# Kernel tuning notes

Hardware: AMD Instinct MI355X
Metric: run time of the kernel (lower is better)

Reference implementation:

```python
import jax, jax.numpy as jnp
import numpy as np

H = 4096        # hidden_size
NH = 32         # num query heads
NKV = 8         # num kv heads
D = H // NH     # head_dim = 128
S = 2048        # num tokens (single causal sequence)
THETA = 1000000.0
SCALE = D ** -0.5


def _rope(x, positions):
    # neox-style (rotate-half) RoPE over full head_dim, as vLLM's get_rope default
    half = D // 2
    inv_freq = 1.0 / (THETA ** (jnp.arange(half, dtype=jnp.float32) / half))
    ang = positions.astype(jnp.float32)[:, None] * inv_freq          # [S, D/2]
    cos = jnp.cos(ang)[:, None, :]                                   # [S, 1, D/2]
    sin = jnp.sin(ang)[:, None, :]
    x1, x2 = x[..., :half], x[..., half:]
    return jnp.concatenate([x1 * cos - x2 * sin, x2 * cos + x1 * sin], axis=-1)


def setup_inputs() -> dict:
    key = jax.random.key(0)
    k1, k2, k3 = jax.random.split(key, 3)
    positions = jnp.arange(S, dtype=jnp.int32)
    hidden_states = jax.random.normal(k1, (S, H), dtype=jnp.float32)
    w_qkv = jax.random.normal(k2, ((NH + 2 * NKV) * D, H), dtype=jnp.float32) * 0.02
    w_o = jax.random.normal(k3, (H, NH * D), dtype=jnp.float32) * 0.02
    return {"positions": positions, "hidden_states": hidden_states,
            "w_qkv": w_qkv, "w_o": w_o}


def reference(positions, hidden_states, w_qkv, w_o):
    # fused QKV projection (Linear, bias=False): x @ W^T
    qkv = hidden_states @ w_qkv.T                                    # [S, (NH+2*NKV)*D]
    q, k, v = jnp.split(qkv, [NH * D, (NH + NKV) * D], axis=-1)
    q = q.reshape(S, NH, D)
    k = k.reshape(S, NKV, D)
    v = v.reshape(S, NKV, D)
    # RoPE on q and k
    q = _rope(q, positions)
    k = _rope(k, positions)
    # GQA causal attention: group NH query heads onto NKV kv heads
    g = NH // NKV
    qg = q.reshape(S, NKV, g, D)
    scores = jnp.einsum('qhgd,khd->hgqk', qg, k) * SCALE             # [NKV, g, S, S]
    causal = positions[:, None] >= positions[None, :]                # [S, S]
    scores = jnp.where(causal[None, None], scores, jnp.float32(-1e30))
    probs = jax.nn.softmax(scores, axis=-1)
    o = jnp.einsum('hgqk,khd->qhgd', probs, v).reshape(S, NH * D)
    return o @ w_o.T                                                 # [S, H]
```

## Files before the change

### kernel.cpp

```cpp
#include <hip/hip_runtime.h>
#include <hip/hip_bf16.h>

#define S_LEN 2048
#define HID 4096
#define NH 32
#define NKV 8
#define DH 128
#define QKV_N ((NH + 2 * NKV) * DH)
#define SCALE_ATT 0.08838834764831845f
#define SCALE2_ATT 0.12751744f

typedef __bf16 bf16;
typedef __bf16 bf16x8 __attribute__((ext_vector_type(8)));
typedef __bf16 bf16x4 __attribute__((ext_vector_type(4)));
typedef float f32x4 __attribute__((ext_vector_type(4)));
typedef float f32x16 __attribute__((ext_vector_type(16)));

__device__ inline f32x4 mfma16(bf16x8 a, bf16x8 b, f32x4 c) {
    return __builtin_amdgcn_mfma_f32_16x16x32_bf16(a, b, c, 0, 0, 0);
}
__device__ inline f32x16 mfma32(bf16x8 a, bf16x8 b, f32x16 c) {
    return __builtin_amdgcn_mfma_f32_32x32x16_bf16(a, b, c, 0, 0, 0);
}

__device__ inline bf16x8 load8(const float* p) {
    const float4 a = ((const float4*)p)[0];
    const float4 b = ((const float4*)p)[1];
    bf16x8 r;
    r[0] = (bf16)a.x; r[1] = (bf16)a.y; r[2] = (bf16)a.z; r[3] = (bf16)a.w;
    r[4] = (bf16)b.x; r[5] = (bf16)b.y; r[6] = (bf16)b.z; r[7] = (bf16)b.w;
    return r;
}
__device__ inline bf16x8 load8(const bf16* p) { return *(const bf16x8*)p; }

__device__ inline void load_lds16(const bf16* g, bf16* lds_base) {
    __builtin_amdgcn_global_load_lds(
        (const __attribute__((address_space(1))) void*)g,
        (__attribute__((address_space(3))) void*)lds_base, 16, 0, 0);
}

__device__ inline unsigned pack2_bf16(float lo, float hi) {
    union { bf16 h[2]; unsigned u; } r;
    r.h[0] = (bf16)lo;
    r.h[1] = (bf16)hi;
    return r.u;
}

__global__ __launch_bounds__(256) void cvt_kernel(const float* __restrict__ src,
                                                  bf16* __restrict__ dst, int n8) {
    int i = blockIdx.x * 256 + threadIdx.x;
    if (i >= n8) return;
    *(bf16x8*)&dst[(size_t)i * 8] = load8(&src[(size_t)i * 8]);
}

template <typename OutT>
__global__ __launch_bounds__(256) void gemm_bt_swz(const bf16* __restrict__ A,
                                                   const bf16* __restrict__ B,
                                                   OutT* __restrict__ C,
                                                   int K, int lda, int ldc) {
    const int tid = threadIdx.x;
    const int lane = tid & 63;
    const int w = tid >> 6;
    const int m0 = blockIdx.y * 128;
    const int n0 = blockIdx.x * 128;
    const int wm = (w >> 1) * 64;
    const int wn = (w & 1) * 64;
    const int ln = lane & 15;
    const int qo = lane >> 4;

    __shared__ bf16 As[128 * 64];
    __shared__ bf16 Bs[128 * 64];

    const int rseg = lane >> 3;
    const int gc = (lane & 7) ^ (rseg & 7);

    f32x4 acc[4][4];
#pragma unroll
    for (int mi = 0; mi < 4; ++mi)
#pragma unroll
        for (int ni = 0; ni < 4; ++ni) acc[mi][ni] = f32x4{0.f, 0.f, 0.f, 0.f};

    for (int k0 = 0; k0 < K; k0 += 64) {
#pragma unroll
        for (int j = 0; j < 4; ++j) {
            const int seg = w * 4 + j;
            const int r = seg * 8 + rseg;
            load_lds16(&A[(size_t)(m0 + r) * lda + k0 + gc * 8], &As[seg * 512]);
            load_lds16(&B[(size_t)(n0 + r) * K + k0 + gc * 8], &Bs[seg * 512]);
        }
        __syncthreads();
#pragma unroll
        for (int kk = 0; kk < 2; ++kk) {
            bf16x8 af[4], bfr[4];
#pragma unroll
            for (int mi = 0; mi < 4; ++mi) {
                const int m = wm + mi * 16 + ln;
                const int sc = (kk * 4 + qo) ^ (ln & 7);
                af[mi] = *(const bf16x8*)&As[m * 64 + sc * 8];
            }
#pragma unroll
            for (int ni = 0; ni < 4; ++ni) {
                const int n = wn + ni * 16 + ln;
                const int sc = (kk * 4 + qo) ^ (ln & 7);
                bfr[ni] = *(const bf16x8*)&Bs[n * 64 + sc * 8];
            }
#pragma unroll
            for (int mi = 0; mi < 4; ++mi)
#pragma unroll
                for (int ni = 0; ni < 4; ++ni)
                    acc[mi][ni] = mfma16(af[mi], bfr[ni], acc[mi][ni]);
        }
        __syncthreads();
    }
#pragma unroll
    for (int mi = 0; mi < 4; ++mi)
#pragma unroll
        for (int ni = 0; ni < 4; ++ni)
#pragma unroll
            for (int r = 0; r < 4; ++r) {
                int row = m0 + wm + mi * 16 + qo * 4 + r;
                int col = n0 + wn + ni * 16 + ln;
                C[(size_t)row * ldc + col] = (OutT)acc[mi][ni][r];
            }
}

template <typename AT, typename OutT>
__global__ __launch_bounds__(256) void gemm_bt(const AT* __restrict__ A,
                                               const float* __restrict__ B,
                                               OutT* __restrict__ C,
                                               int K, int lda, int ldc) {
    const int tid = threadIdx.x;
    const int lane = tid & 63;
    const int w = tid >> 6;
    const int m0 = blockIdx.y * 128;
    const int n0 = blockIdx.x * 128;
    const int wm = (w >> 1) * 64;
    const int wn = (w & 1) * 64;
    const int ln = lane & 15;
    const int qo = lane >> 4;

    __shared__ bf16 As[128 * 72];
    __shared__ bf16 Bs[128 * 72];

    f32x4 acc[4][4];
#pragma unroll
    for (int mi = 0; mi < 4; ++mi)
#pragma unroll
        for (int ni = 0; ni < 4; ++ni) acc[mi][ni] = f32x4{0.f, 0.f, 0.f, 0.f};

    for (int k0 = 0; k0 < K; k0 += 64) {
#pragma unroll
        for (int i = 0; i < 4; ++i) {
            int v = tid + i * 256;
            int row = v >> 3;
            int col = (v & 7) * 8;
            *(bf16x8*)&As[row * 72 + col] = load8(&A[(size_t)(m0 + row) * lda + k0 + col]);
            *(bf16x8*)&Bs[row * 72 + col] = load8(&B[(size_t)(n0 + row) * K + k0 + col]);
        }
        __syncthreads();
#pragma unroll
        for (int kk = 0; kk < 64; kk += 32) {
            bf16x8 af[4], bfr[4];
#pragma unroll
            for (int mi = 0; mi < 4; ++mi)
                af[mi] = *(const bf16x8*)&As[(wm + mi * 16 + ln) * 72 + kk + qo * 8];
#pragma unroll
            for (int ni = 0; ni < 4; ++ni)
                bfr[ni] = *(const bf16x8*)&Bs[(wn + ni * 16 + ln) * 72 + kk + qo * 8];
#pragma unroll
            for (int mi = 0; mi < 4; ++mi)
#pragma unroll
                for (int ni = 0; ni < 4; ++ni)
                    acc[mi][ni] = mfma16(af[mi], bfr[ni], acc[mi][ni]);
        }
        __syncthreads();
    }
#pragma unroll
    for (int mi = 0; mi < 4; ++mi)
#pragma unroll
        for (int ni = 0; ni < 4; ++ni)
#pragma unroll
            for (int r = 0; r < 4; ++r) {
                int row = m0 + wm + mi * 16 + qo * 4 + r;
                int col = n0 + wn + ni * 16 + ln;
                C[(size_t)row * ldc + col] = (OutT)acc[mi][ni][r];
            }
}

__global__ __launch_bounds__(256) void rope_kernel(bf16* __restrict__ qkv,
                                                   const int* __restrict__ positions) {
    int idx = blockIdx.x * 256 + threadIdx.x;
    const int total = S_LEN * (NH + NKV) * 64;
    if (idx >= total) return;
    int d = idx & 63;
    int t = idx >> 6;
    int head = t % (NH + NKV);
    int s = t / (NH + NKV);
    size_t base = (size_t)s * QKV_N + (head < NH ? head * DH : NH * DH + (head - NH) * DH);
    float x1 = (float)qkv[base + d];
    float x2 = (float)qkv[base + d + 64];
    float pos = (float)positions[s];
    float inv = expf(-0.21586735246819178f * (float)d);
    float ang = pos * inv;
    float c = cosf(ang);
    float sn = sinf(ang);
    qkv[base + d] = (bf16)(x1 * c - x2 * sn);
    qkv[base + d + 64] = (bf16)(x2 * c + x1 * sn);
}

__global__ __launch_bounds__(256) void vtrans_kernel(const bf16* __restrict__ qkv,
                                                     bf16* __restrict__ vt_g) {
    const int tid = threadIdx.x;
    const int s0 = blockIdx.x * 64;
    const int kvh = blockIdx.y;
    __shared__ bf16 Ls[64 * 136];
#pragma unroll
    for (int i = 0; i < 4; ++i) {
        int v = tid + i * 256;
        int row = v >> 4;
        int col = (v & 15) * 8;
        *(bf16x8*)&Ls[row * 136 + col] =
            *(const bf16x8*)&qkv[(size_t)(s0 + row) * QKV_N + (NH + NKV) * DH + kvh * DH + col];
    }
    __syncthreads();
#pragma unroll
    for (int i = 0; i < 4; ++i) {
        int u = tid + i * 256;
        int d = u >> 3;
        int sg = (u & 7) * 8;
        bf16x8 r;
#pragma unroll
        for (int j = 0; j < 8; ++j) r[j] = Ls[(sg + j) * 136 + d];
        *(bf16x8*)&vt_g[((size_t)kvh * DH + d) * S_LEN + s0 + sg] = r;
    }
}

__global__ __launch_bounds__(256) void attn_kernel(bf16* __restrict__ qkv,
                                                   const bf16* __restrict__ vt_g) {
    const int tid = threadIdx.x;
    const int lane = tid & 63;
    const int w = tid >> 6;
    const int ln = lane & 31;
    const int hi = lane >> 5;
    const int hq = blockIdx.x;
    const int qtile = (int)gridDim.y - 1 - (int)blockIdx.y;
    const int kvh = hq >> 2;
    const int q0 = qtile * 128;
    const int qrow = q0 + w * 32 + ln;

    __shared__ __align__(128) bf16 Ks[2][64 * 128];
    __shared__ __align__(128) bf16 Vt[2][128 * 64];

    bf16x8 qf[8];
    {
        const bf16* qptr = qkv + (size_t)qrow * QKV_N + hq * DH + hi * 8;
#pragma unroll
        for (int s = 0; s < 8; ++s) qf[s] = *(const bf16x8*)(qptr + s * 16);
    }

    const bf16* ksrc = qkv + NH * DH + kvh * DH;
    const bf16* vsrc = vt_g + (size_t)kvh * DH * S_LEN;
    const int kcK = lane & 15;
    const int krs = lane >> 4;
    const int kcV = lane & 7;
    const int vrs = lane >> 3;

    auto stage = [&](int buf, int kt) {
        const int k0s = kt * 64;
#pragma unroll
        for (int j = 0; j < 4; ++j) {
            int r = w * 16 + j * 4 + krs;
            load_lds16(ksrc + (size_t)(k0s + r) * QKV_N + ((kcK ^ (r & 7)) * 8),
                       &Ks[buf][(w * 16 + j * 4) * 128]);
        }
#pragma unroll
        for (int j = 0; j < 4; ++j) {
            int d = w * 32 + j * 8 + vrs;
            load_lds16(vsrc + (size_t)d * S_LEN + k0s + ((kcV ^ (d & 7)) * 8),
                       &Vt[buf][(w * 32 + j * 8) * 64]);
        }
    };

    f32x16 acc[4];
#pragma unroll
    for (int t = 0; t < 4; ++t)
#pragma unroll
        for (int r = 0; r < 16; ++r) acc[t][r] = 0.f;
    float m2 = -1e30f, l = 0.f;

    const int kt_last = (q0 + 127) >> 6;
    int buf = 0;
    stage(0, 0);
    __syncthreads();

    for (int kt = 0; kt <= kt_last; ++kt) {
        if (kt < kt_last) stage(buf ^ 1, kt + 1);
        const int k0 = kt * 64;
        if (k0 <= q0 + w * 32 + 31) {
            f32x16 st[2];
#pragma unroll
            for (int t = 0; t < 2; ++t)
#pragma unroll
                for (int r = 0; r < 16; ++r) st[t][r] = 0.f;
            const bf16* Kb = &Ks[buf][0];
            __builtin_amdgcn_s_setprio(1);
#pragma unroll
            for (int t = 0; t < 2; ++t) {
                const int key = t * 32 + ln;
#pragma unroll
                for (int s = 0; s < 8; ++s) {
                    bf16x8 kf =
                        *(const bf16x8*)&Kb[key * 128 + (((2 * s + hi) ^ (key & 7)) * 8)];
                    st[t] = mfma32(kf, qf[s], st[t]);
                }
            }
            __builtin_amdgcn_s_setprio(0);
            const bool needMask = (k0 + 63 > q0 + w * 32);
            float tmax = -1e30f;
#pragma unroll
            for (int t = 0; t < 2; ++t)
#pragma unroll
                for (int r = 0; r < 16; ++r) {
                    int kcol = k0 + t * 32 + (r & 3) + 8 * (r >> 2) + 4 * hi;
                    float v = st[t][r] * SCALE2_ATT;
                    if (needMask && kcol > qrow) v = -1e30f;
                    st[t][r] = v;
                    tmax = fmaxf(tmax, v);
                }
            tmax = fmaxf(tmax, __shfl_xor(tmax, 32, 64));
            float mnew = fmaxf(m2, tmax);
            float alpha = exp2f(m2 - mnew);
            float rs = 0.f;
#pragma unroll
            for (int t = 0; t < 2; ++t)
#pragma unroll
                for (int r = 0; r < 16; ++r) {
                    float e = exp2f(st[t][r] - mnew);
                    st[t][r] = e;
                    rs += e;
                }
            rs += __shfl_xor(rs, 32, 64);
            l = l * alpha + rs;
            m2 = mnew;
#pragma unroll
            for (int t = 0; t < 4; ++t)
#pragma unroll
                for (int r = 0; r < 16; ++r) acc[t][r] *= alpha;
            unsigned cw[16];
#pragma unroll
            for (int i = 0; i < 16; ++i)
                cw[i] = pack2_bf16(st[i >> 3][2 * (i & 7)], st[i >> 3][2 * (i & 7) + 1]);
            bf16x8 pa[4];
#pragma unroll
            for (int ks = 0; ks < 4; ++ks) {
                const int base = (ks >> 1) * 8 + (ks & 1) * 4;
                union { unsigned u[4]; bf16x8 v; } pk;
#pragma unroll
                for (int e = 0; e < 2; ++e) {
                    unsigned A = cw[base + e];
                    unsigned B = cw[base + 2 + e];
                    unsigned tA = (unsigned)__shfl_xor((int)A, 32, 64);
                    unsigned tB = (unsigned)__shfl_xor((int)B, 32, 64);
                    pk.u[e] = hi ? tB : A;
                    pk.u[e + 2] = hi ? B : tA;
                }
                pa[ks] = pk.v;
            }
            const bf16* Vb = &Vt[buf][0];
            __builtin_amdgcn_s_setprio(1);
#pragma unroll
            for (int dt = 0; dt < 4; ++dt) {
                const int d = dt * 32 + ln;
#pragma unroll
                for (int ks = 0; ks < 4; ++ks) {
                    bf16x8 vf =
                        *(const bf16x8*)&Vb[d * 64 + (((2 * ks + hi) ^ (d & 7)) * 8)];
                    acc[dt] = mfma32(vf, pa[ks], acc[dt]);
                }
            }
            __builtin_amdgcn_s_setprio(0);
        }
        __syncthreads();
        buf ^= 1;
    }

    const float invl = 1.f / l;
    bf16* outp = qkv + (size_t)qrow * QKV_N + hq * DH;
#pragma unroll
    for (int dt = 0; dt < 4; ++dt)
#pragma unroll
        for (int rq = 0; rq < 4; ++rq) {
            bf16x4 o;
#pragma unroll
            for (int i = 0; i < 4; ++i) o[i] = (bf16)(acc[dt][rq * 4 + i] * invl);
            *(bf16x4*)(outp + dt * 32 + rq * 8 + hi * 4) = o;
        }
}

extern "C" void kernel_launch(void* const* d_in, const int* in_sizes, int n_in,
                              void* d_out, int out_size, void* d_ws, size_t ws_size,
                              hipStream_t stream) {
    const int* positions = (const int*)d_in[0];
    const float* hidden = (const float*)d_in[1];
    const float* w_qkv = (const float*)d_in[2];
    const float* w_o = (const float*)d_in[3];
    float* out = (float*)d_out;

    const size_t n_qkv = (size_t)S_LEN * QKV_N;
    const size_t n_vt = (size_t)NKV * DH * S_LEN;
    const size_t n_hid = (size_t)S_LEN * HID;
    const size_t n_wqkv = (size_t)QKV_N * HID;
    const size_t n_wo = (size_t)HID * HID;

    const size_t need_min = (n_qkv + n_vt) * sizeof(bf16);
    const size_t need_full = (n_qkv + n_vt + n_hid + n_wqkv + n_wo) * sizeof(bf16);
    if (ws_size < need_min) return;

    bf16* qkv = (bf16*)d_ws;
    bf16* vt_g = qkv + n_qkv;
    bf16* hid_b = vt_g + n_vt;
    bf16* wqkv_b = hid_b + n_hid;
    bf16* wo_b = wqkv_b + n_wqkv;
    const bool full = ws_size >= need_full;

    if (full) {
        cvt_kernel<<<(int)(n_hid / 8 + 255) / 256, 256, 0, stream>>>(hidden, hid_b, (int)(n_hid / 8));
        cvt_kernel<<<(int)(n_wqkv / 8 + 255) / 256, 256, 0, stream>>>(w_qkv, wqkv_b, (int)(n_wqkv / 8));
        cvt_kernel<<<(int)(n_wo / 8 + 255) / 256, 256, 0, stream>>>(w_o, wo_b, (int)(n_wo / 8));
        gemm_bt_swz<<<dim3(QKV_N / 128, S_LEN / 128), 256, 0, stream>>>(hid_b, wqkv_b, qkv, HID, HID, QKV_N);
    } else {
        gemm_bt<<<dim3(QKV_N / 128, S_LEN / 128), 256, 0, stream>>>(hidden, w_qkv, qkv, HID, HID, QKV_N);
    }
    const int total = S_LEN * (NH + NKV) * 64;
    rope_kernel<<<(total + 255) / 256, 256, 0, stream>>>(qkv, positions);
    vtrans_kernel<<<dim3(S_LEN / 64, NKV), 256, 0, stream>>>(qkv, vt_g);
    attn_kernel<<<dim3(NH, S_LEN / 128), 256, 0, stream>>>(qkv, vt_g);
    if (full) {
        gemm_bt_swz<<<dim3(HID / 128, S_LEN / 128), 256, 0, stream>>>(qkv, wo_b, out, HID, QKV_N, HID);
    } else {
        gemm_bt<<<dim3(HID / 128, S_LEN / 128), 256, 0, stream>>>(qkv, w_o, out, HID, QKV_N, HID);
    }
}
```

Measured before the change: 551.0 us.

## Replace bf16 GEMMs with larger double-buffered 512-thread 32x32 MFMA kernel

Replaces the 128x128 single-buffered GEMM used for the QKV and output projections with a 256xBN tile kernel of 512 threads. It double-buffers LDS with async global-to-LDS loads and explicit vmcnt waits, uses 32x32x16 MFMAs, and remaps workgroups so neighbouring blocks share data. The intent is to overlap memory loads with MFMA work and raise arithmetic intensity per tile. In exchange it uses much more dynamic LDS (96-128 KB), which may limit occupancy, and the hand-tuned waitcnt counts have to match the number of issued loads.

```diff
diff --git a/kernel.cpp b/kernel.cpp
--- a/kernel.cpp
+++ b/kernel.cpp
@@ -53,74 +53,121 @@
     *(bf16x8*)&dst[(size_t)i * 8] = load8(&src[(size_t)i * 8]);
 }
 
-template <typename OutT>
-__global__ __launch_bounds__(256) void gemm_bt_swz(const bf16* __restrict__ A,
+template <int BN, typename OutT>
+__global__ __launch_bounds__(512, 2) void gemm_8ph(const bf16* __restrict__ A,
                                                    const bf16* __restrict__ B,
                                                    OutT* __restrict__ C,
                                                    int K, int lda, int ldc) {
+    constexpr int WTN = BN / 4;
+    constexpr int NREP = WTN / 32;
+    constexpr int BLOADS = BN / 64;
+    extern __shared__ char smem[];
+    bf16* As = (bf16*)smem;
+    bf16* Bs = (bf16*)(smem + 2 * 256 * 64 * 2);
+
     const int tid = threadIdx.x;
     const int lane = tid & 63;
     const int w = tid >> 6;
-    const int m0 = blockIdx.y * 128;
-    const int n0 = blockIdx.x * 128;
-    const int wm = (w >> 1) * 64;
-    const int wn = (w & 1) * 64;
-    const int ln = lane & 15;
-    const int qo = lane >> 4;
-
-    __shared__ bf16 As[128 * 64];
-    __shared__ bf16 Bs[128 * 64];
-
+    const int wm = w >> 2;
+    const int wn = w & 3;
+    const int ln = lane & 31;
+    const int hi = lane >> 5;
     const int rseg = lane >> 3;
-    const int gc = (lane & 7) ^ (rseg & 7);
-
-    f32x4 acc[4][4];
+    const int gc = (lane & 7) ^ rseg;
+
+    const int nwg = (int)(gridDim.x * gridDim.y);
+    const int wg = (int)(blockIdx.y * gridDim.x + blockIdx.x);
+    const int swz = (wg & 7) * (nwg >> 3) + (wg >> 3);
+    const int tm = swz / (int)gridDim.x;
+    const int tn = swz - tm * (int)gridDim.x;
+    const int m0 = tm * 256;
+    const int n0 = tn * BN;
+
+    const int NT = K >> 6;
+
+    auto stage = [&](int b, int kt) {
+        const int k0 = kt * 64;
+        const bf16* Ag = &A[(size_t)(m0 + w * 32 + rseg) * lda + k0 + gc * 8];
+        bf16* Al = &As[b * (256 * 64) + (w * 32) * 64];
+#pragma unroll
+        for (int j = 0; j < 4; ++j)
+            load_lds16(Ag + (size_t)j * 8 * lda, Al + j * 512);
+        const bf16* Bg = &B[(size_t)(n0 + w * (BN / 8) + rseg) * K + k0 + gc * 8];
+        bf16* Bl = &Bs[b * (BN * 64) + (w * (BN / 8)) * 64];
+#pragma unroll
+        for (int j = 0; j < BLOADS; ++j)
+            load_lds16(Bg + (size_t)j * 8 * K, Bl + j * 512);
+    };
+
+    f32x16 acc[4][NREP];
 #pragma unroll
     for (int mi = 0; mi < 4; ++mi)
 #pragma unroll
-        for (int ni = 0; ni < 4; ++ni) acc[mi][ni] = f32x4{0.f, 0.f, 0.f, 0.f};
-
-    for (int k0 = 0; k0 < K; k0 += 64) {
-#pragma unroll
-        for (int j = 0; j < 4; ++j) {
-            const int seg = w * 4 + j;
-            const int r = seg * 8 + rseg;
-            load_lds16(&A[(size_t)(m0 + r) * lda + k0 + gc * 8], &As[seg * 512]);
-            load_lds16(&B[(size_t)(n0 + r) * K + k0 + gc * 8], &Bs[seg * 512]);
-        }
-        __syncthreads();
-#pragma unroll
-        for (int kk = 0; kk < 2; ++kk) {
-            bf16x8 af[4], bfr[4];
-#pragma unroll
-            for (int mi = 0; mi < 4; ++mi) {
-                const int m = wm + mi * 16 + ln;
-                const int sc = (kk * 4 + qo) ^ (ln & 7);
-                af[mi] = *(const bf16x8*)&As[m * 64 + sc * 8];
-            }
-#pragma unroll
-            for (int ni = 0; ni < 4; ++ni) {
-                const int n = wn + ni * 16 + ln;
-                const int sc = (kk * 4 + qo) ^ (ln & 7);
-                bfr[ni] = *(const bf16x8*)&Bs[n * 64 + sc * 8];
-            }
-#pragma unroll
-            for (int mi = 0; mi < 4; ++mi)
-#pragma unroll
-                for (int ni = 0; ni < 4; ++ni)
-                    acc[mi][ni] = mfma16(af[mi], bfr[ni], acc[mi][ni]);
-        }
-        __syncthreads();
-    }
+        for (int j = 0; j < NREP; ++j)
+#pragma unroll
+            for (int r = 0; r < 16; ++r) acc[mi][j][r] = 0.f;
+
+    stage(0, 0);
+    int buf = 0;
+    for (int kt = 0; kt < NT; ++kt) {
+        if (kt + 1 < NT) {
+            stage(buf ^ 1, kt + 1);
+            if constexpr (BN == 256)
+                asm volatile("s_waitcnt vmcnt(8)" ::: "memory");
+            else
+                asm volatile("s_waitcnt vmcnt(6)" ::: "memory");
+        } else {
+            asm volatile("s_waitcnt vmcnt(0)" ::: "memory");
+        }
+        __builtin_amdgcn_s_barrier();
+        __builtin_amdgcn_sched_barrier(0);
+
+        const bf16* Ab = &As[buf * (256 * 64)];
+        const bf16* Bb = &Bs[buf * (BN * 64)];
+        bf16x8 bfr[NREP][4];
+#pragma unroll
+        for (int j = 0; j < NREP; ++j)
+#pragma unroll
+            for (int kk = 0; kk < 4; ++kk) {
+                const int n = wn * WTN + j * 32 + ln;
+                bfr[j][kk] = *(const bf16x8*)&Bb[n * 64 + (((2 * kk + hi) ^ (ln & 7)) * 8)];
+            }
+#pragma unroll
+        for (int p = 0; p < 2; ++p) {
+            bf16x8 af[2][4];
+#pragma unroll
+            for (int i = 0; i < 2; ++i)
+#pragma unroll
+                for (int kk = 0; kk < 4; ++kk) {
+                    const int m = wm * 128 + (p * 2 + i) * 32 + ln;
+                    af[i][kk] = *(const bf16x8*)&Ab[m * 64 + (((2 * kk + hi) ^ (ln & 7)) * 8)];
+                }
+            __builtin_amdgcn_s_setprio(1);
+#pragma unroll
+            for (int i = 0; i < 2; ++i)
+#pragma unroll
+                for (int j = 0; j < NREP; ++j)
+#pragma unroll
+                    for (int kk = 0; kk < 4; ++kk)
+                        acc[p * 2 + i][j] = mfma32(af[i][kk], bfr[j][kk], acc[p * 2 + i][j]);
+            __builtin_amdgcn_s_setprio(0);
+        }
+        __builtin_amdgcn_sched_barrier(0);
+        asm volatile("s_waitcnt lgkmcnt(0)" ::: "memory");
+        __builtin_amdgcn_s_barrier();
+        __builtin_amdgcn_sched_barrier(0);
+        buf ^= 1;
+    }
+
 #pragma unroll
     for (int mi = 0; mi < 4; ++mi)
 #pragma unroll
-        for (int ni = 0; ni < 4; ++ni)
-#pragma unroll
-            for (int r = 0; r < 4; ++r) {
-                int row = m0 + wm + mi * 16 + qo * 4 + r;
-                int col = n0 + wn + ni * 16 + ln;
-                C[(size_t)row * ldc + col] = (OutT)acc[mi][ni][r];
+        for (int j = 0; j < NREP; ++j)
+#pragma unroll
+            for (int r = 0; r < 16; ++r) {
+                int row = m0 + wm * 128 + mi * 32 + (r & 3) + 8 * (r >> 2) + 4 * hi;
+                int col = n0 + wn * WTN + j * 32 + ln;
+                C[(size_t)row * ldc + col] = (OutT)acc[mi][j][r];
             }
 }
 
@@ -427,7 +474,10 @@
         cvt_kernel<<<(int)(n_hid / 8 + 255) / 256, 256, 0, stream>>>(hidden, hid_b, (int)(n_hid / 8));
         cvt_kernel<<<(int)(n_wqkv / 8 + 255) / 256, 256, 0, stream>>>(w_qkv, wqkv_b, (int)(n_wqkv / 8));
         cvt_kernel<<<(int)(n_wo / 8 + 255) / 256, 256, 0, stream>>>(w_o, wo_b, (int)(n_wo / 8));
-        gemm_bt_swz<<<dim3(QKV_N / 128, S_LEN / 128), 256, 0, stream>>>(hid_b, wqkv_b, qkv, HID, HID, QKV_N);
+        hipFuncSetAttribute(reinterpret_cast<const void*>(&gemm_8ph<256, bf16>),
+                            hipFuncAttributeMaxDynamicSharedMemorySize, 131072);
+        gemm_8ph<256, bf16><<<dim3(QKV_N / 256, S_LEN / 256), 512, 131072, stream>>>(
+            hid_b, wqkv_b, qkv, HID, HID, QKV_N);
     } else {
         gemm_bt<<<dim3(QKV_N / 128, S_LEN / 128), 256, 0, stream>>>(hidden, w_qkv, qkv, HID, HID, QKV_N);
     }
@@ -436,7 +486,10 @@
     vtrans_kernel<<<dim3(S_LEN / 64, NKV), 256, 0, stream>>>(qkv, vt_g);
     attn_kernel<<<dim3(NH, S_LEN / 128), 256, 0, stream>>>(qkv, vt_g);
     if (full) {
-        gemm_bt_swz<<<dim3(HID / 128, S_LEN / 128), 256, 0, stream>>>(qkv, wo_b, out, HID, QKV_N, HID);
+        hipFuncSetAttribute(reinterpret_cast<const void*>(&gemm_8ph<128, float>),
+                            hipFuncAttributeMaxDynamicSharedMemorySize, 98304);
+        gemm_8ph<128, float><<<dim3(HID / 128, S_LEN / 256), 512, 98304, stream>>>(
+            qkv, wo_b, out, HID, QKV_N, HID);
     } else {
         gemm_bt<<<dim3(HID / 128, S_LEN / 128), 256, 0, stream>>>(qkv, w_o, out, HID, QKV_N, HID);
     }
```

After: 576.7 us. 4.7% more time.
